# Performance work log

Measured on AMD Instinct MI355X. Metric: run time of the kernel, lower is better.

Reference implementation:

```python
import jax, jax.numpy as jnp
import numpy as np

N_NODES = 50000
N_EDGES = 800000
DIM = 128
N_LAYERS = 4
EPS = 1e-5  # BatchNorm1d default eps


def setup_inputs() -> dict:
    key = jax.random.key(0)
    k_x, k_e, k_w = jax.random.split(key, 3)
    x = jax.random.normal(k_x, (N_NODES, DIM), dtype=jnp.float32)
    edge_index = jax.random.randint(k_e, (2, N_EDGES), 0, N_NODES, dtype=jnp.int32)
    # stacked per-layer params (input_dim == hidden_dim == DIM)
    Ws = jax.random.normal(k_w, (N_LAYERS, DIM, DIM), dtype=jnp.float32) * (1.0 / np.sqrt(DIM))
    bs = jnp.zeros((N_LAYERS, DIM), jnp.float32)
    gammas = jnp.ones((N_LAYERS, DIM), jnp.float32)
    betas = jnp.zeros((N_LAYERS, DIM), jnp.float32)
    return {"x": x, "edge_index": edge_index, "Ws": Ws, "bs": bs,
            "gammas": gammas, "betas": betas}


def gcn_conv(x, W, b, src, dst, n):
    # PyG GCNConv: h = X W; out = D^{-1/2}(A+I)D^{-1/2} h + b
    h = x @ W                                       # [N, D]
    deg = jnp.zeros((n,), h.dtype).at[dst].add(1.0) + 1.0  # +1 self-loop
    dis = jax.lax.rsqrt(deg)                        # deg > 0 due to self-loops
    msg = h[src] * (dis[src] * dis[dst])[:, None]   # [E, D] gather + scale
    out = jnp.zeros_like(h).at[dst].add(msg)        # scatter-add aggregate
    out = out + h * (dis * dis)[:, None]            # self-loop term, norm = 1/deg
    return out + b


def batchnorm(z, gamma, beta):
    # BatchNorm1d training-mode math: batch mean, biased variance
    mu = z.mean(axis=0)
    var = z.var(axis=0)
    return (z - mu) * jax.lax.rsqrt(var + EPS) * gamma + beta


def reference(x, edge_index, Ws, bs, gammas, betas):
    src, dst = edge_index[0], edge_index[1]
    z = x
    for i in range(N_LAYERS):
        z = gcn_conv(z, Ws[i], bs[i], src, dst, z.shape[0])
        z = jax.nn.relu(z)
        z = batchnorm(z, gammas[i], betas[i])
        # Dropout: identity (eval mode / deterministic reference)
    return z
```

## Files before the change

### kernel.cpp

```cpp
#include <hip/hip_runtime.h>

#define N_NODES 50000
#define N_EDGES 800000
#define DIM 128
#define NLAYERS 4
#define BN_EPS 1e-5f
#define SCAN_BLOCKS 196
#define WSTRIDE 136

typedef __attribute__((ext_vector_type(8))) short short8;
typedef __attribute__((ext_vector_type(4))) float f32x4;

__device__ __forceinline__ float bf2f(unsigned short u){
    union { unsigned int i; float f; } x; x.i = ((unsigned int)u) << 16; return x.f;
}
__device__ __forceinline__ unsigned short f2bf(float f){
    union { float f; unsigned int i; } x; x.f = f;
    unsigned int lsb = (x.i >> 16) & 1u;
    unsigned int r = x.i + 0x7fffu + lsb;
    return (unsigned short)(r >> 16);
}


__global__ __launch_bounds__(256) void k_zero(int* __restrict__ p, int n){
    int i = blockIdx.x * 256 + threadIdx.x;
    if (i < n) p[i] = 0;
}

__global__ __launch_bounds__(256) void k_count(const int* __restrict__ dst,
                                               int* __restrict__ degcnt){
    int e = blockIdx.x * 256 + threadIdx.x;
    if (e < N_EDGES) atomicAdd(&degcnt[dst[e]], 1);
}

__global__ __launch_bounds__(256) void k_dis(const int* __restrict__ degcnt,
                                             float* __restrict__ dis){
    int i = blockIdx.x * 256 + threadIdx.x;
    if (i < N_NODES) dis[i] = rsqrtf((float)degcnt[i] + 1.0f);
}

__global__ __launch_bounds__(256) void k_scan1(const int* __restrict__ degcnt,
                                               int* __restrict__ rowptr,
                                               int* __restrict__ bsum){
    __shared__ int tmp[256];
    int t = threadIdx.x;
    int i = blockIdx.x * 256 + t;
    int v = (i < N_NODES) ? degcnt[i] : 0;
    tmp[t] = v;
    __syncthreads();
    #pragma unroll
    for (int off = 1; off < 256; off <<= 1){
        int u = (t >= off) ? tmp[t - off] : 0;
        __syncthreads();
        tmp[t] += u;
        __syncthreads();
    }
    if (i < N_NODES) rowptr[i] = tmp[t] - v;
    if (t == 255) bsum[blockIdx.x] = tmp[255];
}

__global__ __launch_bounds__(256) void k_scan2(int* __restrict__ bsum){
    __shared__ int tmp[256];
    int t = threadIdx.x;
    int v = (t < SCAN_BLOCKS) ? bsum[t] : 0;
    tmp[t] = v;
    __syncthreads();
    #pragma unroll
    for (int off = 1; off < 256; off <<= 1){
        int u = (t >= off) ? tmp[t - off] : 0;
        __syncthreads();
        tmp[t] += u;
        __syncthreads();
    }
    if (t < SCAN_BLOCKS) bsum[t] = tmp[t] - v;
}

__global__ __launch_bounds__(256) void k_scan3(const int* __restrict__ bsum,
                                               int* __restrict__ rowptr,
                                               int* __restrict__ wptr){
    int i = blockIdx.x * 256 + threadIdx.x;
    if (i < N_NODES){
        int r = rowptr[i] + bsum[blockIdx.x];
        rowptr[i] = r; wptr[i] = r;
    }
    if (i == 0) rowptr[N_NODES] = N_EDGES;
}

__global__ __launch_bounds__(256) void k_fill(const int* __restrict__ src,
                                              const int* __restrict__ dst,
                                              const float* __restrict__ dis,
                                              int* __restrict__ wptr,
                                              int2* __restrict__ epair){
    int e = blockIdx.x * 256 + threadIdx.x;
    if (e < N_EDGES){
        int s = src[e], d = dst[e];
        float w = dis[s] * dis[d];
        int p = atomicAdd(&wptr[d], 1);
        int2 pr; pr.x = s; pr.y = __float_as_int(w);
        epair[p] = pr;
    }
}

__global__ __launch_bounds__(256) void k_cvt(const float* __restrict__ x,
                                             unsigned short* __restrict__ xg){
    int i = blockIdx.x * 256 + threadIdx.x;
    if (i >= N_NODES * 16) return;
    int row = i >> 4;
    int c = (i & 15) * 8;
    float4 v0 = *(const float4*)&x[row*DIM + c];
    float4 v1 = *(const float4*)&x[row*DIM + c + 4];
    int g = c >> 5, wi = c & 31;
    ushort4 o0, o1;
    o0.x = f2bf(v0.x); o0.y = f2bf(v0.y); o0.z = f2bf(v0.z); o0.w = f2bf(v0.w);
    o1.x = f2bf(v1.x); o1.y = f2bf(v1.y); o1.z = f2bf(v1.z); o1.w = f2bf(v1.w);
    unsigned short* p = &xg[(size_t)g*N_NODES*32 + (size_t)row*32 + wi];
    *(ushort4*)p = o0;
    *(ushort4*)(p + 4) = o1;
}

template<bool HAS>
__global__ __launch_bounds__(256) void k_wprep(const float* __restrict__ W,
                                               const float* __restrict__ scsh,
                                               unsigned short* __restrict__ wthi,
                                               unsigned short* __restrict__ wtlo){
    int idx = blockIdx.x * 256 + threadIdx.x;
    int c = idx >> 7, k = idx & 127;
    float v = W[k*DIM + c];
    if (HAS) v *= scsh[k];
    unsigned short hi = f2bf(v);
    float lo = v - bf2f(hi);
    wthi[c*DIM + k] = hi;
    wtlo[c*DIM + k] = f2bf(lo);
}

template<bool HAS>
__global__ __launch_bounds__(128) void k_wbias(const float* __restrict__ W,
                                               const float* __restrict__ scsh,
                                               float* __restrict__ bias2){
    int c = threadIdx.x;
    float acc = 0.f;
    if (HAS){
        #pragma unroll 4
        for (int k = 0; k < DIM; k++)
            acc = fmaf(scsh[DIM + k], W[k*DIM + c], acc);
    }
    bias2[c] = acc;
}


__global__ __launch_bounds__(256) void k_gemm(const unsigned short* __restrict__ zg,
                                              const unsigned short* __restrict__ wthi,
                                              const unsigned short* __restrict__ wtlo,
                                              const float* __restrict__ bias2,
                                              unsigned short* __restrict__ hb){
    __shared__ short whi[DIM * WSTRIDE];
    __shared__ short wlo[DIM * WSTRIDE];
    int tid = threadIdx.x;

    {
        const uint4* gh = (const uint4*)wthi;
        const uint4* gl = (const uint4*)wtlo;
        #pragma unroll
        for (int it = 0; it < 8; it++){
            int ch = tid + 256*it;
            int c = ch >> 4, k8 = ch & 15;
            int off = c*WSTRIDE + k8*8;
            *(uint4*)&whi[off] = gh[ch];
            *(uint4*)&wlo[off] = gl[ch];
        }
    }
    __syncthreads();

    int lane = tid & 63;
    int wv   = tid >> 6;
    int m = lane & 15;
    int q = lane >> 4;
    int row0 = blockIdx.x * 64 + wv * 16;
    int arow = row0 + m;
    bool avalid = arow < N_NODES;

    f32x4 acc[8];
    #pragma unroll
    for (int t = 0; t < 8; t++) acc[t] = (f32x4){0.f, 0.f, 0.f, 0.f};

    #pragma unroll
    for (int g = 0; g < 4; g++){
        short8 a = {0,0,0,0,0,0,0,0};
        if (avalid)
            a = *(const short8*)&zg[(size_t)g*N_NODES*32 + (size_t)arow*32 + q*8];
        #pragma unroll
        for (int t = 0; t < 8; t++){
            int col = t*16 + m;
            int off = col*WSTRIDE + g*32 + q*8;
            short8 bh = *(const short8*)&whi[off];
            short8 bl = *(const short8*)&wlo[off];
            acc[t] = __builtin_amdgcn_mfma_f32_16x16x32_bf16(a, bh, acc[t], 0, 0, 0);
            acc[t] = __builtin_amdgcn_mfma_f32_16x16x32_bf16(a, bl, acc[t], 0, 0, 0);
        }
    }

    #pragma unroll
    for (int t = 0; t < 8; t++){
        int colg = t*16 + m;
        float bz = bias2[colg];
        size_t base = (size_t)(t >> 1)*N_NODES*32 + (t & 1)*16 + m;
        #pragma unroll
        for (int r = 0; r < 4; r++){
            int row = row0 + q*4 + r;
            if (row < N_NODES)
                hb[base + (size_t)row*32] = f2bf(acc[t][r] + bz);
        }
    }
}

__global__ __launch_bounds__(256) void k_agg(const unsigned short* __restrict__ h,
                                             const int* __restrict__ rowptr,
                                             const int2* __restrict__ epair,
                                             const float* __restrict__ dis,
                                             const float* __restrict__ bias,
                                             unsigned short* __restrict__ out,
                                             float* __restrict__ stats){
    int lane = threadIdx.x & 63;
    int w    = threadIdx.x >> 6;
    int g    = blockIdx.x & 3;
    int sub  = lane >> 4;
    int cp   = lane & 15;
    const ushort2* hg = (const ushort2*)(h + (size_t)g * N_NODES * 32);
    ushort2* og = (ushort2*)(out + (size_t)g * N_NODES * 32);
    float b0 = bias[g*32 + 2*cp], b1 = bias[g*32 + 2*cp + 1];
    float s0 = 0.f, s1 = 0.f, q0 = 0.f, q1 = 0.f;
    int bg = blockIdx.x >> 2;
    int nstride = (gridDim.x >> 2) * 4;

    for (int node = bg*4 + w; node < N_NODES; node += nstride){
        float di = dis[node];
        int e0 = rowptr[node], e1 = rowptr[node + 1];
        float pa0 = 0.f, pa1 = 0.f, pb0 = 0.f, pb1 = 0.f;
        float pc0 = 0.f, pc1 = 0.f, pd0 = 0.f, pd1 = 0.f;
        if (sub == 0){
            ushort2 hv = hg[node*16 + cp];
            float dii = di * di;
            pa0 = bf2f(hv.x) * dii; pa1 = bf2f(hv.y) * dii;
        }
        int e = e0;
        for (; e + 16 <= e1; e += 16){
            int2 P0 = epair[e + sub];
            int2 P1 = epair[e + 4 + sub];
            int2 P2 = epair[e + 8 + sub];
            int2 P3 = epair[e + 12 + sub];
            ushort2 X0 = hg[P0.x*16 + cp];
            ushort2 X1 = hg[P1.x*16 + cp];
            ushort2 X2 = hg[P2.x*16 + cp];
            ushort2 X3 = hg[P3.x*16 + cp];
            float w0 = __int_as_float(P0.y), w1 = __int_as_float(P1.y);
            float w2 = __int_as_float(P2.y), w3 = __int_as_float(P3.y);
            pa0 = fmaf(bf2f(X0.x), w0, pa0); pa1 = fmaf(bf2f(X0.y), w0, pa1);
            pb0 = fmaf(bf2f(X1.x), w1, pb0); pb1 = fmaf(bf2f(X1.y), w1, pb1);
            pc0 = fmaf(bf2f(X2.x), w2, pc0); pc1 = fmaf(bf2f(X2.y), w2, pc1);
            pd0 = fmaf(bf2f(X3.x), w3, pd0); pd1 = fmaf(bf2f(X3.y), w3, pd1);
        }
        for (; e + 8 <= e1; e += 8){
            int2 P0 = epair[e + sub];
            int2 P1 = epair[e + 4 + sub];
            ushort2 X0 = hg[P0.x*16 + cp];
            ushort2 X1 = hg[P1.x*16 + cp];
            float w0 = __int_as_float(P0.y), w1 = __int_as_float(P1.y);
            pa0 = fmaf(bf2f(X0.x), w0, pa0); pa1 = fmaf(bf2f(X0.y), w0, pa1);
            pb0 = fmaf(bf2f(X1.x), w1, pb0); pb1 = fmaf(bf2f(X1.y), w1, pb1);
        }
        for (; e < e1; e += 4){
            int ide = e + sub;
            int2 pr = (ide < e1) ? epair[ide] : make_int2(0, 0);
            ushort2 xv = hg[pr.x*16 + cp];
            float we = __int_as_float(pr.y);
            pa0 = fmaf(bf2f(xv.x), we, pa0);
            pa1 = fmaf(bf2f(xv.y), we, pa1);
        }
        float r0 = (pa0 + pb0) + (pc0 + pd0);
        float r1 = (pa1 + pb1) + (pc1 + pd1);
        r0 += __shfl_xor(r0, 16); r1 += __shfl_xor(r1, 16);
        r0 += __shfl_xor(r0, 32); r1 += __shfl_xor(r1, 32);
        if (sub == 0){
            float a0 = fmaxf(r0 + b0, 0.f);
            float a1 = fmaxf(r1 + b1, 0.f);
            ushort2 ov; ov.x = f2bf(a0); ov.y = f2bf(a1);
            og[node*16 + cp] = ov;
            s0 += a0; s1 += a1; q0 += a0*a0; q1 += a1*a1;
        }
    }

    __shared__ float red[4][16][4];
    if (sub == 0){
        red[w][cp][0] = s0; red[w][cp][1] = s1;
        red[w][cp][2] = q0; red[w][cp][3] = q1;
    }
    __syncthreads();
    if (w == 0 && sub == 0){
        #pragma unroll
        for (int ww = 1; ww < 4; ww++){
            s0 += red[ww][cp][0]; s1 += red[ww][cp][1];
            q0 += red[ww][cp][2]; q1 += red[ww][cp][3];
        }
        int c = g*32 + 2*cp;
        atomicAdd(&stats[c],         s0);
        atomicAdd(&stats[c + 1],     s1);
        atomicAdd(&stats[DIM + c],     q0);
        atomicAdd(&stats[DIM + c + 1], q1);
    }
}

__global__ void k_bnstat(const float* __restrict__ stats,
                         const float* __restrict__ gamma,
                         const float* __restrict__ beta,
                         float* __restrict__ scsh){
    int c = threadIdx.x;
    float mu  = stats[c] * (1.0f / N_NODES);
    float var = stats[DIM + c] * (1.0f / N_NODES) - mu * mu;
    float sc  = rsqrtf(var + BN_EPS) * gamma[c];
    scsh[c] = sc;
    scsh[DIM + c] = beta[c] - mu * sc;
}

__global__ __launch_bounds__(256) void k_bn(const uint4* __restrict__ in,
                                            const float* __restrict__ scsh,
                                            float4* __restrict__ outf){
    int i = blockIdx.x * 256 + threadIdx.x;
    if (i >= N_NODES * DIM / 8) return;
    int row = i >> 4;
    int c = (i * 8) & (DIM - 1);
    int gg = c >> 5, wi = c & 31;
    uint4 raw = in[gg*(N_NODES*4) + row*4 + (wi >> 3)];
    float4 sc0 = *(const float4*)&scsh[c];
    float4 sc1 = *(const float4*)&scsh[c + 4];
    float4 sh0 = *(const float4*)&scsh[DIM + c];
    float4 sh1 = *(const float4*)&scsh[DIM + c + 4];
    unsigned int u[4] = {raw.x, raw.y, raw.z, raw.w};
    float v[8];
    #pragma unroll
    for (int j = 0; j < 4; j++){
        v[2*j]   = bf2f((unsigned short)(u[j] & 0xffff));
        v[2*j+1] = bf2f((unsigned short)(u[j] >> 16));
    }
    float4 r0, r1;
    r0.x = fmaf(v[0], sc0.x, sh0.x);
    r0.y = fmaf(v[1], sc0.y, sh0.y);
    r0.z = fmaf(v[2], sc0.z, sh0.z);
    r0.w = fmaf(v[3], sc0.w, sh0.w);
    r1.x = fmaf(v[4], sc1.x, sh1.x);
    r1.y = fmaf(v[5], sc1.y, sh1.y);
    r1.z = fmaf(v[6], sc1.z, sh1.z);
    r1.w = fmaf(v[7], sc1.w, sh1.w);
    outf[2*i]   = r0;
    outf[2*i+1] = r1;
}


extern "C" void kernel_launch(void* const* d_in, const int* in_sizes, int n_in,
                              void* d_out, int out_size, void* d_ws, size_t ws_size,
                              hipStream_t stream){
    const float* x   = (const float*)d_in[0];
    const int*   src = (const int*)d_in[1];
    const int*   dst = src + N_EDGES;
    const float* Ws  = (const float*)d_in[2];
    const float* bs  = (const float*)d_in[3];
    const float* gs  = (const float*)d_in[4];
    const float* be  = (const float*)d_in[5];

    char* w = (char*)d_ws;
    int*   degcnt = (int*)(w);
    float* stats  = (float*)(w + 200000);
    float* scsh   = (float*)(w + 204096);
    float* dis    = (float*)(w + 208192);
    int*   rowptr = (int*)(w + 408192);
    int*   wptr   = (int*)(w + 608208);
    int*   bsum   = (int*)(w + 808208);
    float* bias2  = (float*)(w + 809232);
    unsigned short* wthi = (unsigned short*)(w + 809744);
    unsigned short* wtlo = (unsigned short*)(w + 842512);
    int2*  epair  = (int2*)(w + 875280);
    unsigned short* xg   = (unsigned short*)(w + 7275280);
    unsigned short* bufA = (unsigned short*)(w + 20075280);
    unsigned short* hb   = (unsigned short*)(w + 32875280);

    k_zero<<<(51024 + 255)/256, 256, 0, stream>>>(degcnt, 51024);
    k_count<<<3125, 256, 0, stream>>>(dst, degcnt);
    k_dis<<<196, 256, 0, stream>>>(degcnt, dis);
    k_scan1<<<SCAN_BLOCKS, 256, 0, stream>>>(degcnt, rowptr, bsum);
    k_scan2<<<1, 256, 0, stream>>>(bsum);
    k_scan3<<<SCAN_BLOCKS, 256, 0, stream>>>(bsum, rowptr, wptr);
    k_fill<<<3125, 256, 0, stream>>>(src, dst, dis, wptr, epair);
    k_cvt<<<3125, 256, 0, stream>>>(x, xg);

    for (int L = 0; L < NLAYERS; L++){
        const float* Wl = Ws + L*DIM*DIM;
        if (L == 0){
            k_wprep<false><<<64, 256, 0, stream>>>(Wl, nullptr, wthi, wtlo);
            k_wbias<false><<<1, 128, 0, stream>>>(Wl, nullptr, bias2);
        } else {
            k_wprep<true><<<64, 256, 0, stream>>>(Wl, scsh + (L-1)*256, wthi, wtlo);
            k_wbias<true><<<1, 128, 0, stream>>>(Wl, scsh + (L-1)*256, bias2);
        }
        const unsigned short* zin = (L == 0) ? xg : bufA;
        k_gemm<<<(N_NODES + 63)/64, 256, 0, stream>>>(zin, wthi, wtlo, bias2, hb);
        k_agg<<<2048, 256, 0, stream>>>(hb, rowptr, epair, dis, bs + L*DIM,
                                        bufA, stats + L*256);
        k_bnstat<<<1, 128, 0, stream>>>(stats + L*256, gs + L*DIM, be + L*DIM,
                                        scsh + L*256);
    }
    k_bn<<<3125, 256, 0, stream>>>((const uint4*)bufA, scsh + 3*256,
                                   (float4*)d_out);
}
```

Measured before the change: 613.5 us.

## Fuse small prep kernels, convert fp32 input inside GEMM, prefetch next node in aggregation

Folds the dis computation into scan1 and merges the weight-bias kernel into wprep as an extra block, which drops several tiny launches per run. The first-layer GEMM now reads the fp32 input and converts it to bf16 in registers, removing the separate conversion pass and its intermediate buffer. The aggregation loop software-prefetches the next node's rowptr, self feature and dis while processing the current node, to hide load latency. The trade-off is uncoalesced-ish fp32 reads in the layer-0 GEMM and more live registers in the aggregation loop.

```diff
diff --git a/kernel.cpp b/kernel.cpp
--- a/kernel.cpp
+++ b/kernel.cpp
@@ -33,19 +33,15 @@
     if (e < N_EDGES) atomicAdd(&degcnt[dst[e]], 1);
 }
 
-__global__ __launch_bounds__(256) void k_dis(const int* __restrict__ degcnt,
-                                             float* __restrict__ dis){
-    int i = blockIdx.x * 256 + threadIdx.x;
-    if (i < N_NODES) dis[i] = rsqrtf((float)degcnt[i] + 1.0f);
-}
-
 __global__ __launch_bounds__(256) void k_scan1(const int* __restrict__ degcnt,
                                                int* __restrict__ rowptr,
-                                               int* __restrict__ bsum){
+                                               int* __restrict__ bsum,
+                                               float* __restrict__ dis){
     __shared__ int tmp[256];
     int t = threadIdx.x;
     int i = blockIdx.x * 256 + t;
     int v = (i < N_NODES) ? degcnt[i] : 0;
+    if (i < N_NODES) dis[i] = rsqrtf((float)v + 1.0f);
     tmp[t] = v;
     __syncthreads();
     #pragma unroll
@@ -101,54 +97,41 @@
     }
 }
 
-__global__ __launch_bounds__(256) void k_cvt(const float* __restrict__ x,
-                                             unsigned short* __restrict__ xg){
-    int i = blockIdx.x * 256 + threadIdx.x;
-    if (i >= N_NODES * 16) return;
-    int row = i >> 4;
-    int c = (i & 15) * 8;
-    float4 v0 = *(const float4*)&x[row*DIM + c];
-    float4 v1 = *(const float4*)&x[row*DIM + c + 4];
-    int g = c >> 5, wi = c & 31;
-    ushort4 o0, o1;
-    o0.x = f2bf(v0.x); o0.y = f2bf(v0.y); o0.z = f2bf(v0.z); o0.w = f2bf(v0.w);
-    o1.x = f2bf(v1.x); o1.y = f2bf(v1.y); o1.z = f2bf(v1.z); o1.w = f2bf(v1.w);
-    unsigned short* p = &xg[(size_t)g*N_NODES*32 + (size_t)row*32 + wi];
-    *(ushort4*)p = o0;
-    *(ushort4*)(p + 4) = o1;
-}
-
 template<bool HAS>
 __global__ __launch_bounds__(256) void k_wprep(const float* __restrict__ W,
                                                const float* __restrict__ scsh,
                                                unsigned short* __restrict__ wthi,
-                                               unsigned short* __restrict__ wtlo){
-    int idx = blockIdx.x * 256 + threadIdx.x;
-    int c = idx >> 7, k = idx & 127;
-    float v = W[k*DIM + c];
-    if (HAS) v *= scsh[k];
-    unsigned short hi = f2bf(v);
-    float lo = v - bf2f(hi);
-    wthi[c*DIM + k] = hi;
-    wtlo[c*DIM + k] = f2bf(lo);
-}
-
-template<bool HAS>
-__global__ __launch_bounds__(128) void k_wbias(const float* __restrict__ W,
-                                               const float* __restrict__ scsh,
+                                               unsigned short* __restrict__ wtlo,
                                                float* __restrict__ bias2){
-    int c = threadIdx.x;
-    float acc = 0.f;
-    if (HAS){
-        #pragma unroll 4
-        for (int k = 0; k < DIM; k++)
-            acc = fmaf(scsh[DIM + k], W[k*DIM + c], acc);
-    }
-    bias2[c] = acc;
-}
-
-
-__global__ __launch_bounds__(256) void k_gemm(const unsigned short* __restrict__ zg,
+    int tid = threadIdx.x;
+    if (blockIdx.x < 64){
+        int idx = blockIdx.x * 256 + tid;
+        int c = idx >> 7, k = idx & 127;
+        float v = W[k*DIM + c];
+        if (HAS) v *= scsh[k];
+        unsigned short hi = f2bf(v);
+        float lo = v - bf2f(hi);
+        wthi[c*DIM + k] = hi;
+        wtlo[c*DIM + k] = f2bf(lo);
+    } else {
+        __shared__ float part[256];
+        int c = tid >> 1, half = tid & 1;
+        float acc = 0.f;
+        if (HAS){
+            int k0 = half * 64;
+            #pragma unroll 4
+            for (int k = k0; k < k0 + 64; k++)
+                acc = fmaf(scsh[DIM + k], W[k*DIM + c], acc);
+        }
+        part[tid] = acc;
+        __syncthreads();
+        if (half == 0) bias2[c] = part[2*c] + part[2*c + 1];
+    }
+}
+
+
+template<int MODE>
+__global__ __launch_bounds__(256) void k_gemm(const void* __restrict__ zraw,
                                               const unsigned short* __restrict__ wthi,
                                               const unsigned short* __restrict__ wtlo,
                                               const float* __restrict__ bias2,
@@ -186,8 +169,20 @@
     #pragma unroll
     for (int g = 0; g < 4; g++){
         short8 a = {0,0,0,0,0,0,0,0};
-        if (avalid)
-            a = *(const short8*)&zg[(size_t)g*N_NODES*32 + (size_t)arow*32 + q*8];
+        if (avalid){
+            if (MODE == 0){
+                const float* xp = (const float*)zraw + (size_t)arow*DIM + g*32 + q*8;
+                float4 v0 = *(const float4*)xp;
+                float4 v1 = *(const float4*)(xp + 4);
+                a[0] = (short)f2bf(v0.x); a[1] = (short)f2bf(v0.y);
+                a[2] = (short)f2bf(v0.z); a[3] = (short)f2bf(v0.w);
+                a[4] = (short)f2bf(v1.x); a[5] = (short)f2bf(v1.y);
+                a[6] = (short)f2bf(v1.z); a[7] = (short)f2bf(v1.w);
+            } else {
+                a = *(const short8*)((const unsigned short*)zraw
+                      + (size_t)g*N_NODES*32 + (size_t)arow*32 + q*8);
+            }
+        }
         #pragma unroll
         for (int t = 0; t < 8; t++){
             int col = t*16 + m;
@@ -232,13 +227,33 @@
     int bg = blockIdx.x >> 2;
     int nstride = (gridDim.x >> 2) * 4;
 
-    for (int node = bg*4 + w; node < N_NODES; node += nstride){
-        float di = dis[node];
-        int e0 = rowptr[node], e1 = rowptr[node + 1];
+    int node = bg*4 + w;
+    int ne0 = 0, ne1 = 0;
+    ushort2 nhv; nhv.x = 0; nhv.y = 0;
+    float ndi = 0.f;
+    if (node < N_NODES){
+        ne0 = rowptr[node];
+        ne1 = rowptr[node + 1];
+        nhv = hg[node*16 + cp];
+        ndi = dis[node];
+    }
+
+    while (node < N_NODES){
+        int e0 = ne0, e1 = ne1;
+        ushort2 hv = nhv;
+        float di = ndi;
+
+        int nnext = node + nstride;
+        if (nnext < N_NODES){
+            ne0 = rowptr[nnext];
+            ne1 = rowptr[nnext + 1];
+            nhv = hg[nnext*16 + cp];
+            ndi = dis[nnext];
+        }
+
         float pa0 = 0.f, pa1 = 0.f, pb0 = 0.f, pb1 = 0.f;
         float pc0 = 0.f, pc1 = 0.f, pd0 = 0.f, pd1 = 0.f;
         if (sub == 0){
-            ushort2 hv = hg[node*16 + cp];
             float dii = di * di;
             pa0 = bf2f(hv.x) * dii; pa1 = bf2f(hv.y) * dii;
         }
@@ -287,6 +302,7 @@
             og[node*16 + cp] = ov;
             s0 += a0; s1 += a1; q0 += a0*a0; q1 += a1*a1;
         }
+        node = nnext;
     }
 
     __shared__ float red[4][16][4];
@@ -378,30 +394,28 @@
     unsigned short* wthi = (unsigned short*)(w + 809744);
     unsigned short* wtlo = (unsigned short*)(w + 842512);
     int2*  epair  = (int2*)(w + 875280);
-    unsigned short* xg   = (unsigned short*)(w + 7275280);
-    unsigned short* bufA = (unsigned short*)(w + 20075280);
-    unsigned short* hb   = (unsigned short*)(w + 32875280);
+    unsigned short* bufA = (unsigned short*)(w + 7275280);
+    unsigned short* hb   = (unsigned short*)(w + 20075280);
 
     k_zero<<<(51024 + 255)/256, 256, 0, stream>>>(degcnt, 51024);
     k_count<<<3125, 256, 0, stream>>>(dst, degcnt);
-    k_dis<<<196, 256, 0, stream>>>(degcnt, dis);
-    k_scan1<<<SCAN_BLOCKS, 256, 0, stream>>>(degcnt, rowptr, bsum);
+    k_scan1<<<SCAN_BLOCKS, 256, 0, stream>>>(degcnt, rowptr, bsum, dis);
     k_scan2<<<1, 256, 0, stream>>>(bsum);
     k_scan3<<<SCAN_BLOCKS, 256, 0, stream>>>(bsum, rowptr, wptr);
     k_fill<<<3125, 256, 0, stream>>>(src, dst, dis, wptr, epair);
-    k_cvt<<<3125, 256, 0, stream>>>(x, xg);
 
     for (int L = 0; L < NLAYERS; L++){
         const float* Wl = Ws + L*DIM*DIM;
         if (L == 0){
-            k_wprep<false><<<64, 256, 0, stream>>>(Wl, nullptr, wthi, wtlo);
-            k_wbias<false><<<1, 128, 0, stream>>>(Wl, nullptr, bias2);
+            k_wprep<false><<<65, 256, 0, stream>>>(Wl, nullptr, wthi, wtlo, bias2);
+            k_gemm<0><<<(N_NODES + 63)/64, 256, 0, stream>>>(x, wthi, wtlo,
+                                                             bias2, hb);
         } else {
-            k_wprep<true><<<64, 256, 0, stream>>>(Wl, scsh + (L-1)*256, wthi, wtlo);
-            k_wbias<true><<<1, 128, 0, stream>>>(Wl, scsh + (L-1)*256, bias2);
-        }
-        const unsigned short* zin = (L == 0) ? xg : bufA;
-        k_gemm<<<(N_NODES + 63)/64, 256, 0, stream>>>(zin, wthi, wtlo, bias2, hb);
+            k_wprep<true><<<65, 256, 0, stream>>>(Wl, scsh + (L-1)*256,
+                                                  wthi, wtlo, bias2);
+            k_gemm<1><<<(N_NODES + 63)/64, 256, 0, stream>>>(bufA, wthi, wtlo,
+                                                             bias2, hb);
+        }
         k_agg<<<2048, 256, 0, stream>>>(hb, rowptr, epair, dis, bs + L*DIM,
                                         bufA, stats + L*256);
         k_bnstat<<<1, 128, 0, stream>>>(stats + L*256, gs + L*DIM, be + L*DIM,
```

New measurement: 595.4 us. 1.03x faster.
